# Kernel tuning notes

Measured on AMD Instinct MI355X. Metric: run time of the kernel, lower is better.

Reference implementation:

```python
import jax, jax.numpy as jnp
import numpy as np

N_SAMPLES = 2 ** 15          # 32768
STEP = 256                   # transform_step_size
WIN = 2048                   # transform/synthesis window
N_FRAMES = N_SAMPLES // STEP # 128
N_COEFFS = WIN // 2 + 1      # 1025
DILATIONS = (1, 2, 4, 8, 16, 32, 64, 1)


def hann(n):
    return 0.5 - 0.5 * jnp.cos(2.0 * jnp.pi * jnp.arange(n, dtype=jnp.float32) / n)


def transform(audio):
    # audio: (B, 1, N) -> magnitude STFT (B, 1024, 128)
    x = audio[:, 0, :]
    x = jnp.pad(x, ((0, 0), (0, WIN - STEP)))  # pad so n_frames == N_SAMPLES // STEP
    idx = np.arange(N_FRAMES)[:, None] * STEP + np.arange(WIN)[None, :]
    frames = x[:, idx] * hann(WIN)
    spec = jnp.abs(jnp.fft.rfft(frames, norm='ortho'))   # (B, F, 1025)
    return spec[..., : N_COEFFS - 1].transpose(0, 2, 1)  # (B, 1024, F)


def conv1x1(x, w, b):
    # x: (B, I, T), w: (O, I, 1), b: (O,)
    return jnp.einsum('oi,bit->bot', w[:, :, 0], x) + b[None, :, None]


def anticausal_block(x, w, b, dilation):
    # kernel_size=2 anti-causal dilated conv: looks at t and t+dilation (pad future)
    x_fut = jnp.pad(x, ((0, 0), (0, 0), (0, dilation)))[:, :, dilation:]
    y = (jnp.einsum('oi,bit->bot', w[:, :, 0], x)
         + jnp.einsum('oi,bit->bot', w[:, :, 1], x_fut)
         + b[None, :, None])
    y = jax.nn.leaky_relu(y, 0.2)
    y = y + x
    # do_norm: per-example max-norm
    y = y / (jnp.max(jnp.abs(y), axis=(1, 2), keepdims=True) + 1e-8)
    return y


def upsample_with_holes(x, desired_size):
    # zero-stuffing upsample: out[..., ::step] = x
    b, c, t = x.shape
    step = desired_size // t
    out = jnp.zeros((b, c, desired_size), x.dtype)
    return out.at[:, :, ::step].set(x)


def freq_domain_resonance(coeffs):
    # coeffs: (1, C, 1025) in [0, 1); per-frame decay = repeated spectral multiply
    c = jnp.clip(coeffs, 0.0, 0.9999)
    exps = jnp.arange(1, N_FRAMES + 1, dtype=coeffs.dtype)
    mags = c[:, :, None, :] ** exps[None, None, :, None]     # (1, C, F, 1025)
    frames = jnp.fft.irfft(mags, n=WIN) * hann(WIN)
    hop = WIN // 2
    total = hop * (N_FRAMES - 1) + WIN
    idx = np.arange(N_FRAMES)[:, None] * hop + np.arange(WIN)[None, :]
    out = jnp.zeros(frames.shape[:2] + (total,), frames.dtype)
    out = out.at[:, :, idx].add(frames)                      # overlap-add
    return out[..., :N_SAMPLES]                              # (1, C, N)


def fft_convolve(a, b):
    # circular-free conv via zero-padding to 2N, keep first N (matches repo fft_convolve)
    n = a.shape[-1]
    spec = jnp.fft.rfft(a, n=2 * n) * jnp.fft.rfft(b, n=2 * n)
    return jnp.fft.irfft(spec, n=2 * n)[..., :n]


def reference(audio, proj_in_w, proj_in_b, blocks_w, blocks_b,
              proj_sparse_w, proj_sparse_b, proj_dense_w, proj_dense_b, resonances):
    spec = transform(audio)                         # (B, 1024, 128)
    h = conv1x1(spec, proj_in_w, proj_in_b)         # (B, 32, 128)
    acc = jnp.zeros_like(h)
    for i, d in enumerate(DILATIONS):               # fixed 8-block stack
        h = anticausal_block(h, blocks_w[i], blocks_b[i], d)
        acc = acc + h
    x = conv1x1(acc, proj_sparse_w, proj_sparse_b)  # (B, 256, 128)
    sparse = jax.nn.relu(x)
    x = conv1x1(sparse, proj_dense_w, proj_dense_b) # (B, 32, 128)
    x = upsample_with_holes(x, N_SAMPLES)           # (B, 32, 32768)
    res = freq_domain_resonance(resonances)         # (1, 32, 32768), broadcast over B
    y = fft_convolve(x, res)                        # (B, 32, 32768)
    y = jnp.sum(y, axis=1, keepdims=True)           # (B, 1, 32768)
    return y, sparse


def setup_inputs() -> dict:
    key = jax.random.key(0)
    ks = jax.random.split(key, 12)
    u = lambda k, shape: jax.random.uniform(k, shape, jnp.float32, -0.05, 0.05)
    return {
        'audio': jax.random.normal(ks[0], (32, 1, N_SAMPLES), jnp.float32),
        'proj_in_w': u(ks[1], (32, 1024, 1)),
        'proj_in_b': jnp.zeros((32,), jnp.float32),
        'blocks_w': u(ks[2], (8, 32, 32, 2)),
        'blocks_b': jnp.zeros((8, 32), jnp.float32),
        'proj_sparse_w': u(ks[3], (256, 32, 1)),
        'proj_sparse_b': jnp.zeros((256,), jnp.float32),
        'proj_dense_w': u(ks[4], (32, 256, 1)),
        'proj_dense_b': jnp.zeros((32,), jnp.float32),
        'resonances': jax.random.uniform(ks[5], (1, 32, N_COEFFS), jnp.float32, 0.0, 1.0),
    }
```

## Files before the change

kernel.cpp:

```cpp
#include <hip/hip_runtime.h>

#define PI_F 3.14159265358979323846f

typedef short bf16x8 __attribute__((ext_vector_type(8)));
typedef float f32x4 __attribute__((ext_vector_type(4)));

#define MFMA16(acc, a, b) \
  acc = __builtin_amdgcn_mfma_f32_16x16x32_bf16(a, b, acc, 0, 0, 0)

#define WS_SPEC   0u
#define WS_H0     4194304u
#define WS_ACC    4325376u
#define WS_V      4456448u
#define WS_WTIN   4587520u
#define WS_WST    4620288u
#define WS_WDT    4628480u
#define WS_FRAMES 4636672u
#define WS_RES    6733824u

__device__ __forceinline__ void fft2048_stages(float2* buf, int tid) {
  for (int stage = 0; stage < 11; ++stage) {
    int half = 1 << stage;
    float base = -PI_F / (float)half;
    for (int t = tid; t < 1024; t += 256) {
      int j  = t & (half - 1);
      int i0 = ((t >> stage) << (stage + 1)) + j;
      int i1 = i0 + half;
      float s, c;
      __sincosf(base * (float)j, &s, &c);
      float2 u = buf[i0];
      float2 w = buf[i1];
      float tr = c * w.x - s * w.y;
      float ti = c * w.y + s * w.x;
      buf[i0] = make_float2(u.x + tr, u.y + ti);
      buf[i1] = make_float2(u.x - tr, u.y - ti);
    }
    __syncthreads();
  }
}

__global__ __launch_bounds__(256) void k_fft(const float* __restrict__ audio,
                                             const float* __restrict__ resin,
                                             float* __restrict__ spec,
                                             float* __restrict__ frames) {
  __shared__ float2 buf[2048];
  int blk = blockIdx.x;
  if (blk < 2048) {
    int b  = blk >> 6;
    int f0 = (blk & 63) * 2;
    for (int j = threadIdx.x; j < 2048; j += 256) {
      float h = 0.5f - 0.5f * __cosf(0.0030679615757712823f * (float)j);
      int i1 = f0 * 256 + j;
      int i2 = i1 + 256;
      float a1 = (i1 < 32768) ? audio[b * 32768 + i1] : 0.f;
      float a2 = (i2 < 32768) ? audio[b * 32768 + i2] : 0.f;
      buf[__brev((unsigned)j) >> 21] = make_float2(a1 * h, a2 * h);
    }
    __syncthreads();
    fft2048_stages(buf, threadIdx.x);
    const float scale = 0.5f * 0.022097086912079608f;
    for (int k = threadIdx.x; k < 1024; k += 256) {
      float2 zk = buf[k];
      float2 zn = buf[(2048 - k) & 2047];
      float f1r = zk.x + zn.x, f1i = zk.y - zn.y;
      float f2r = zk.y + zn.y, f2i = zk.x - zn.x;
      spec[(b * 128 + f0) * 1024 + k]     = sqrtf(f1r * f1r + f1i * f1i) * scale;
      spec[(b * 128 + f0 + 1) * 1024 + k] = sqrtf(f2r * f2r + f2i * f2i) * scale;
    }
  } else {
    int r = blk - 2048;
    int c = r >> 4;
    int g = r & 15;
    float e1 = (float)(2 * g + 1);
    for (int k = threadIdx.x; k < 2048; k += 256) {
      int kk = (k <= 1024) ? k : 2048 - k;
      float cv = resin[c * 1025 + kk];
      cv = fminf(fmaxf(cv, 0.f), 0.9999f);
      float m1 = __powf(cv, e1);
      float m2 = m1 * cv;
      buf[__brev((unsigned)k) >> 21] = make_float2(m1, m2);
    }
    __syncthreads();
    fft2048_stages(buf, threadIdx.x);
    for (int j = threadIdx.x; j < 2048; j += 256) {
      float h  = 0.5f - 0.5f * __cosf(0.0030679615757712823f * (float)j);
      float sc = h * (1.f / 2048.f);
      float2 z = buf[j];
      frames[(c * 32 + 2 * g) * 2048 + j]     = z.x * sc;
      frames[(c * 32 + 2 * g + 1) * 2048 + j] = z.y * sc;
    }
  }
}

__global__ __launch_bounds__(256) void k_prep(const float* __restrict__ Win,
                                              const float* __restrict__ Ws,
                                              const float* __restrict__ Wd,
                                              const float* __restrict__ bwIn,
                                              float* __restrict__ WT,
                                              float* __restrict__ WsT,
                                              float* __restrict__ WdT,
                                              short* __restrict__ Whg,
                                              short* __restrict__ Wlg) {
  int i = blockIdx.x * 256 + threadIdx.x;
  if (i < 32768) { int o = i >> 10, k = i & 1023; WT[k * 32 + o] = Win[i]; }
  if (i < 8192)  { int o2 = i >> 5, m = i & 31;   WsT[m * 256 + o2] = Ws[i]; }
  if (i < 8192)  { int c = i >> 8, o2 = i & 255;  WdT[o2 * 32 + c] = Wd[i]; }
  if (i < 16384) {
    int w = i & 1, m = (i >> 1) & 31, o = (i >> 6) & 31, s = i >> 11;
    float val = bwIn[i];
    unsigned bits = __float_as_uint(val);
    float rem = val - __uint_as_float(bits & 0xffff0000u);
    int row = (s * 2 + w) * 32 + o;
    Whg[row * 32 + m] = (short)(bits >> 16);
    Wlg[row * 32 + m] = (short)(__float_as_uint(rem) >> 16);
  }
}

__global__ __launch_bounds__(256) void k_proj_in(const float* __restrict__ spec,
                                                 const float* __restrict__ WT,
                                                 const float* __restrict__ bias,
                                                 float* __restrict__ h0) {
  __shared__ float specL[8][1024];
  __shared__ float red[32][8][8];
  int b  = blockIdx.x >> 4;
  int t0 = (blockIdx.x & 15) * 8;
  for (int i = threadIdx.x; i < 8192; i += 256) {
    int tt = i >> 10, k = i & 1023;
    specL[tt][k] = spec[(b * 128 + t0 + tt) * 1024 + k];
  }
  __syncthreads();
  int o = threadIdx.x & 31, p = threadIdx.x >> 5;
  float part[8] = {0.f,0.f,0.f,0.f,0.f,0.f,0.f,0.f};
  for (int i = 0; i < 128; ++i) {
    int k = p * 128 + ((i + p * 4) & 127);
    float w = WT[k * 32 + o];
#pragma unroll
    for (int tt = 0; tt < 8; ++tt) part[tt] += w * specL[tt][k];
  }
#pragma unroll
  for (int tt = 0; tt < 8; ++tt) red[o][tt][p] = part[tt];
  __syncthreads();
  int oo = threadIdx.x >> 3, tt2 = threadIdx.x & 7;
  float s = bias[oo];
#pragma unroll
  for (int p2 = 0; p2 < 8; ++p2) s += red[oo][tt2][p2];
  h0[b * 4096 + oo * 128 + t0 + tt2] = s;
}

__global__ __launch_bounds__(1024) void k_chain(const float* __restrict__ h0,
                                                const short* __restrict__ Whg,
                                                const short* __restrict__ Wlg,
                                                const float* __restrict__ bb,
                                                float* __restrict__ accout) {
  __shared__ __align__(16) short Hh[192 * 40];
  __shared__ __align__(16) short Hl[192 * 40];
  __shared__ float Hf[128 * 33];
  __shared__ float bL[256];
  __shared__ float red[16];
  int b = blockIdx.x, tid = threadIdx.x;

  for (int i = tid; i < 4096; i += 1024) {
    int t = i & 127;
    int o = i >> 7;
    float val = h0[b * 4096 + i];
    Hf[t * 33 + o] = val;
    unsigned bits = __float_as_uint(val);
    float rem = val - __uint_as_float(bits & 0xffff0000u);
    Hh[t * 40 + o] = (short)(bits >> 16);
    Hl[t * 40 + o] = (short)(__float_as_uint(rem) >> 16);
  }
  for (int i = tid; i < 64 * 40; i += 1024) {
    Hh[128 * 40 + i] = 0;
    Hl[128 * 40 + i] = 0;
  }
  if (tid < 256) bL[tid] = bb[tid];
  __syncthreads();

  int wave = tid >> 6, lane = tid & 63;
  int quad = lane >> 4, l15 = lane & 15;
  int t0 = (wave & 7) * 16, o0 = (wave >> 3) * 16;
  int tD = t0 + quad * 4;
  int oD = o0 + l15;

  const bf16x8* Hh8 = (const bf16x8*)Hh;
  const bf16x8* Hl8 = (const bf16x8*)Hl;
  const bf16x8* Wh8 = (const bf16x8*)Whg;
  const bf16x8* Wl8 = (const bf16x8*)Wlg;

  float accsum[4] = {0.f, 0.f, 0.f, 0.f};
  const int DIL[8] = {1, 2, 4, 8, 16, 32, 64, 1};

#pragma unroll
  for (int s = 0; s < 8; ++s) {
    int arow = t0 + l15;
    int frow = arow + DIL[s];
    bf16x8 Ah = Hh8[arow * 5 + quad];
    bf16x8 Al = Hl8[arow * 5 + quad];
    bf16x8 Fh = Hh8[frow * 5 + quad];
    bf16x8 Fl = Hl8[frow * 5 + quad];
    int w0row = ((s * 2 + 0) * 32 + oD) * 4 + quad;
    int w1row = ((s * 2 + 1) * 32 + oD) * 4 + quad;
    bf16x8 B0h = Wh8[w0row], B0l = Wl8[w0row];
    bf16x8 B1h = Wh8[w1row], B1l = Wl8[w1row];
    float bias = bL[s * 32 + oD];
    f32x4 acc = {bias, bias, bias, bias};
    MFMA16(acc, Ah, B0h); MFMA16(acc, Ah, B0l); MFMA16(acc, Al, B0h);
    MFMA16(acc, Fh, B1h); MFMA16(acc, Fh, B1l); MFMA16(acc, Fl, B1h);
    float hnew[4], lmax = 0.f;
#pragma unroll
    for (int r = 0; r < 4; ++r) {
      float sv = acc[r];
      sv = (sv > 0.f) ? sv : 0.2f * sv;
      sv += Hf[(tD + r) * 33 + oD];
      hnew[r] = sv;
      lmax = fmaxf(lmax, fabsf(sv));
    }
#pragma unroll
    for (int off = 32; off > 0; off >>= 1)
      lmax = fmaxf(lmax, __shfl_down(lmax, off, 64));
    if (lane == 0) red[wave] = lmax;
    __syncthreads();
    float mx = red[0];
#pragma unroll
    for (int i = 1; i < 16; ++i) mx = fmaxf(mx, red[i]);
    float nm = 1.f / (mx + 1e-8f);
#pragma unroll
    for (int r = 0; r < 4; ++r) {
      float hv = hnew[r] * nm;
      accsum[r] += hv;
      int t = tD + r;
      Hf[t * 33 + oD] = hv;
      unsigned bits = __float_as_uint(hv);
      float rem = hv - __uint_as_float(bits & 0xffff0000u);
      Hh[t * 40 + oD] = (short)(bits >> 16);
      Hl[t * 40 + oD] = (short)(__float_as_uint(rem) >> 16);
    }
    __syncthreads();
  }
#pragma unroll
  for (int r = 0; r < 4; ++r)
    accout[b * 4096 + (tD + r) * 32 + oD] = accsum[r];
}

__global__ __launch_bounds__(256) void k_sparse_dense(const float* __restrict__ acc,
                                                      const float* __restrict__ WsT,
                                                      const float* __restrict__ bs,
                                                      const float* __restrict__ WdT,
                                                      const float* __restrict__ bd,
                                                      float* __restrict__ out_sparse,
                                                      float* __restrict__ v) {
  __shared__ float accL[32];
  __shared__ float sL[256];
  __shared__ float red[8][32];
  int b = blockIdx.x >> 7, t = blockIdx.x & 127;
  int tid = threadIdx.x;
  if (tid < 32) accL[tid] = acc[b * 4096 + t * 32 + tid];
  __syncthreads();
  float s = bs[tid];
  for (int m = 0; m < 32; ++m) s += WsT[m * 256 + tid] * accL[m];
  s = fmaxf(s, 0.f);
  out_sparse[b * 32768 + tid * 128 + t] = s;
  sL[tid] = s;
  __syncthreads();
  int c = tid & 31, p = tid >> 5;
  float part = 0.f;
  for (int j = 0; j < 32; ++j) {
    int o2 = p * 32 + j;
    part += WdT[o2 * 32 + c] * sL[o2];
  }
  red[p][c] = part;
  __syncthreads();
  if (tid < 32) {
    float vv = bd[tid];
    for (int p2 = 0; p2 < 8; ++p2) vv += red[p2][tid];
    v[b * 4096 + tid * 128 + t] = vv;
  }
}

__global__ __launch_bounds__(256) void k_res_assemble(const float* __restrict__ frames,
                                                      float* __restrict__ res) {
  int i = blockIdx.x * 256 + threadIdx.x;
  int c = i >> 15, s = i & 32767;
  int g = s >> 10, j0 = s & 1023;
  float v = frames[(c * 32 + g) * 2048 + j0];
  if (g > 0) v += frames[(c * 32 + g - 1) * 2048 + j0 + 1024];
  res[i] = v;
}

__global__ __launch_bounds__(256) void k_bpack(const float* __restrict__ res,
                                               short* __restrict__ Bh,
                                               short* __restrict__ Bl) {
  int c = blockIdx.x >> 4, o = blockIdx.x & 15;
  int r = threadIdx.x;
  bf16x8 hv, lv;
#pragma unroll
  for (int j = 0; j < 8; ++j) {
    float val = res[c * 32768 + (8 * o + j) * 256 + r];
    unsigned bits = __float_as_uint(val);
    float rem = val - __uint_as_float(bits & 0xffff0000u);
    hv[j] = (short)(bits >> 16);
    lv[j] = (short)(__float_as_uint(rem) >> 16);
  }
  int unit = (blockIdx.x * 16 + (r >> 4)) * 16 + (r & 15);
  ((bf16x8*)Bh)[unit] = hv;
  ((bf16x8*)Bl)[unit] = lv;
}

__global__ __launch_bounds__(256, 2) void k_conv(const float* __restrict__ v,
                                                 const short* __restrict__ Bh,
                                                 const short* __restrict__ Bl,
                                                 float* __restrict__ y) {
  __shared__ __align__(16) short AH[2 * 32 * 264];
  __shared__ __align__(16) short AL[2 * 32 * 264];
  __shared__ float vwin[2][2][16][48];

  int blk = blockIdx.x;
  int b2 = blk / 20;
  int e  = blk - b2 * 20;
  int j, uc;
  if      (e < 2)  { j = 0; uc = e; }
  else if (e < 6)  { j = 1; uc = e - 2; }
  else if (e < 12) { j = 2; uc = e - 6; }
  else             { j = 3; uc = e - 12; }
  int D0 = 32 * j - 16 * uc;

  for (int i = threadIdx.x; i < 3008; i += 256) {
    int ii = i % 47;
    int r  = i / 47;
    int c  = r & 15, p = (r >> 4) & 1, bbv = r >> 5;
    int d  = D0 - 15 + ii;
    vwin[bbv][p][c][ii] = (d >= 0 && d < 128)
        ? v[(2 * b2 + bbv) * 4096 + (16 * p + c) * 128 + d] : 0.f;
  }
  __syncthreads();

  int lane = threadIdx.x & 63, wave = threadIdx.x >> 6;
  int quad = lane >> 4, l15 = lane & 15;
  int cq   = quad >> 1;
  int og   = 2 * uc + (quad & 1);
  int nt0  = wave * 4;

  f32x4 acc[4][4];
#pragma unroll
  for (int a = 0; a < 4; ++a)
#pragma unroll
    for (int t = 0; t < 4; ++t) acc[a][t] = (f32x4)0.f;

  const bf16x8* AH8 = (const bf16x8*)AH;
  const bf16x8* AL8 = (const bf16x8*)AL;
  const bf16x8* Bh8 = (const bf16x8*)Bh;
  const bf16x8* Bl8 = (const bf16x8*)Bl;
  short2* AH2 = (short2*)AH;
  short2* AL2 = (short2*)AL;

  int abase[4];
#pragma unroll
  for (int bbi = 0; bbi < 2; ++bbi)
#pragma unroll
    for (int qs = 0; qs < 2; ++qs)
      abase[bbi * 2 + qs] = (bbi * 32 + qs * 16 + l15) * 33 + quad;

  for (int p = 0; p < 2; ++p) {
    for (int i = threadIdx.x; i < 8192; i += 256) {
      int kk2 = i & 127;
      int row = (i >> 7) & 31;
      int bbv = i >> 12;
      int cl  = kk2 >> 3;
      int uu  = (kk2 & 7) * 2;
      int ii  = row - uu + 15;
      float v0 = vwin[bbv][p][cl][ii];
      float v1 = vwin[bbv][p][cl][ii - 1];
      unsigned w0 = __float_as_uint(v0), w1 = __float_as_uint(v1);
      float r0 = v0 - __uint_as_float(w0 & 0xffff0000u);
      float r1 = v1 - __uint_as_float(w1 & 0xffff0000u);
      int u2 = (bbv * 32 + row) * 132 + kk2;
      AH2[u2] = make_short2((short)(w0 >> 16), (short)(w1 >> 16));
      AL2[u2] = make_short2((short)(__float_as_uint(r0) >> 16),
                            (short)(__float_as_uint(r1) >> 16));
    }
    __syncthreads();

#pragma unroll
    for (int ks = 0; ks < 8; ++ks) {
      bf16x8 ah[4], al[4];
#pragma unroll
      for (int tl = 0; tl < 4; ++tl) {
        ah[tl] = AH8[abase[tl] + ks * 4];
        al[tl] = AL8[abase[tl] + ks * 4];
      }
      int c = 16 * p + 2 * ks + cq;
      int bb0 = (c * 16 + og) * 256 + l15;
#pragma unroll
      for (int t = 0; t < 4; ++t) {
        int bi = bb0 + (nt0 + t) * 16;
        bf16x8 bvh = Bh8[bi];
        bf16x8 bvl = Bl8[bi];
#pragma unroll
        for (int tl = 0; tl < 4; ++tl) {
          MFMA16(acc[tl][t], ah[tl], bvh);
          MFMA16(acc[tl][t], ah[tl], bvl);
          MFMA16(acc[tl][t], al[tl], bvh);
        }
      }
    }
    __syncthreads();
  }

#pragma unroll
  for (int bbi = 0; bbi < 2; ++bbi)
#pragma unroll
    for (int qs = 0; qs < 2; ++qs) {
      float* yb = y + (2 * b2 + bbi) * 32768
                    + (32 * j + qs * 16 + quad * 4) * 256 + l15;
#pragma unroll
      for (int t = 0; t < 4; ++t)
#pragma unroll
        for (int reg = 0; reg < 4; ++reg)
          atomicAdd(yb + reg * 256 + (nt0 + t) * 16, acc[bbi * 2 + qs][t][reg]);
    }
}

extern "C" void kernel_launch(void* const* d_in, const int* in_sizes, int n_in,
                              void* d_out, int out_size, void* d_ws, size_t ws_size,
                              hipStream_t stream) {
  const float* audio = (const float*)d_in[0];
  const float* Win   = (const float*)d_in[1];
  const float* bin   = (const float*)d_in[2];
  const float* bw    = (const float*)d_in[3];
  const float* bb    = (const float*)d_in[4];
  const float* Ws    = (const float*)d_in[5];
  const float* bs    = (const float*)d_in[6];
  const float* Wd    = (const float*)d_in[7];
  const float* bd    = (const float*)d_in[8];
  const float* reson = (const float*)d_in[9];

  float* out = (float*)d_out;
  float* ws  = (float*)d_ws;

  float* spec   = ws + WS_SPEC;
  float* h0     = ws + WS_H0;
  float* accb   = ws + WS_ACC;
  float* vbuf   = ws + WS_V;
  float* WT     = ws + WS_WTIN;
  float* WsT    = ws + WS_WST;
  float* WdT    = ws + WS_WDT;
  float* frames = ws + WS_FRAMES;
  float* resbuf = ws + WS_RES;
  short* Bh = (short*)(ws + WS_FRAMES);
  short* Bl = (short*)(ws + WS_FRAMES + 524288u);
  short* Whg = (short*)(ws + WS_V);
  short* Wlg = (short*)(ws + WS_V + 8192u);

  hipMemsetAsync(d_out, 0, 1048576u * sizeof(float), stream);

  k_prep<<<128, 256, 0, stream>>>(Win, Ws, Wd, bw, WT, WsT, WdT, Whg, Wlg);
  k_fft<<<2560, 256, 0, stream>>>(audio, reson, spec, frames);
  k_res_assemble<<<4096, 256, 0, stream>>>(frames, resbuf);
  k_bpack<<<512, 256, 0, stream>>>(resbuf, Bh, Bl);
  k_proj_in<<<512, 256, 0, stream>>>(spec, WT, bin, h0);
  k_chain<<<32, 1024, 0, stream>>>(h0, Whg, Wlg, bb, accb);
  k_sparse_dense<<<4096, 256, 0, stream>>>(accb, WsT, bs, WdT, bd, out + 1048576, vbuf);
  k_conv<<<320, 256, 0, stream>>>(vbuf, Bh, Bl, out);
}
```

Baseline: 215.2 us.

## Split k_conv per batch with 8 waves and smaller per-wave tiles

Each k_conv block now handles one batch element instead of a pair, using 512 threads where each wave computes a 2x2 MFMA tile instead of 4x4. The grid doubles to 640 blocks, and LDS and register use per block drop, to raise occupancy and parallelism across CUs. The trade-off is that each B fragment loaded from global memory is reused across fewer A tiles and fewer batches, so B traffic per FLOP doubles and the number of atomic adds stays about the same.

```diff
diff --git a/kernel.cpp b/kernel.cpp
--- a/kernel.cpp
+++ b/kernel.cpp
@@ -306,17 +306,17 @@
   ((bf16x8*)Bl)[unit] = lv;
 }
 
-__global__ __launch_bounds__(256, 2) void k_conv(const float* __restrict__ v,
+__global__ __launch_bounds__(512, 4) void k_conv(const float* __restrict__ v,
                                                  const short* __restrict__ Bh,
                                                  const short* __restrict__ Bl,
                                                  float* __restrict__ y) {
-  __shared__ __align__(16) short AH[2 * 32 * 264];
-  __shared__ __align__(16) short AL[2 * 32 * 264];
-  __shared__ float vwin[2][2][16][48];
+  __shared__ __align__(16) short AH[32 * 264];
+  __shared__ __align__(16) short AL[32 * 264];
+  __shared__ float vwin[2][16][48];
 
   int blk = blockIdx.x;
-  int b2 = blk / 20;
-  int e  = blk - b2 * 20;
+  int b = blk / 20;
+  int e = blk - b * 20;
   int j, uc;
   if      (e < 2)  { j = 0; uc = e; }
   else if (e < 6)  { j = 1; uc = e - 2; }
@@ -324,13 +324,13 @@
   else             { j = 3; uc = e - 12; }
   int D0 = 32 * j - 16 * uc;
 
-  for (int i = threadIdx.x; i < 3008; i += 256) {
+  for (int i = threadIdx.x; i < 1504; i += 512) {
     int ii = i % 47;
     int r  = i / 47;
-    int c  = r & 15, p = (r >> 4) & 1, bbv = r >> 5;
+    int c  = r & 15, p = r >> 4;
     int d  = D0 - 15 + ii;
-    vwin[bbv][p][c][ii] = (d >= 0 && d < 128)
-        ? v[(2 * b2 + bbv) * 4096 + (16 * p + c) * 128 + d] : 0.f;
+    vwin[p][c][ii] = (d >= 0 && d < 128)
+        ? v[b * 4096 + (16 * p + c) * 128 + d] : 0.f;
   }
   __syncthreads();
 
@@ -338,13 +338,10 @@
   int quad = lane >> 4, l15 = lane & 15;
   int cq   = quad >> 1;
   int og   = 2 * uc + (quad & 1);
-  int nt0  = wave * 4;
-
-  f32x4 acc[4][4];
-#pragma unroll
-  for (int a = 0; a < 4; ++a)
-#pragma unroll
-    for (int t = 0; t < 4; ++t) acc[a][t] = (f32x4)0.f;
+  int nt0  = wave * 2;
+
+  f32x4 acc00 = (f32x4)0.f, acc01 = (f32x4)0.f;
+  f32x4 acc10 = (f32x4)0.f, acc11 = (f32x4)0.f;
 
   const bf16x8* AH8 = (const bf16x8*)AH;
   const bf16x8* AL8 = (const bf16x8*)AL;
@@ -353,27 +350,22 @@
   short2* AH2 = (short2*)AH;
   short2* AL2 = (short2*)AL;
 
-  int abase[4];
-#pragma unroll
-  for (int bbi = 0; bbi < 2; ++bbi)
-#pragma unroll
-    for (int qs = 0; qs < 2; ++qs)
-      abase[bbi * 2 + qs] = (bbi * 32 + qs * 16 + l15) * 33 + quad;
+  int abase0 = (0 * 16 + l15) * 33 + quad;
+  int abase1 = (1 * 16 + l15) * 33 + quad;
 
   for (int p = 0; p < 2; ++p) {
-    for (int i = threadIdx.x; i < 8192; i += 256) {
+    for (int i = threadIdx.x; i < 4096; i += 512) {
       int kk2 = i & 127;
-      int row = (i >> 7) & 31;
-      int bbv = i >> 12;
+      int row = i >> 7;
       int cl  = kk2 >> 3;
       int uu  = (kk2 & 7) * 2;
       int ii  = row - uu + 15;
-      float v0 = vwin[bbv][p][cl][ii];
-      float v1 = vwin[bbv][p][cl][ii - 1];
+      float v0 = vwin[p][cl][ii];
+      float v1 = vwin[p][cl][ii - 1];
       unsigned w0 = __float_as_uint(v0), w1 = __float_as_uint(v1);
       float r0 = v0 - __uint_as_float(w0 & 0xffff0000u);
       float r1 = v1 - __uint_as_float(w1 & 0xffff0000u);
-      int u2 = (bbv * 32 + row) * 132 + kk2;
+      int u2 = row * 132 + kk2;
       AH2[u2] = make_short2((short)(w0 >> 16), (short)(w1 >> 16));
       AL2[u2] = make_short2((short)(__float_as_uint(r0) >> 16),
                             (short)(__float_as_uint(r1) >> 16));
@@ -382,42 +374,35 @@
 
 #pragma unroll
     for (int ks = 0; ks < 8; ++ks) {
-      bf16x8 ah[4], al[4];
-#pragma unroll
-      for (int tl = 0; tl < 4; ++tl) {
-        ah[tl] = AH8[abase[tl] + ks * 4];
-        al[tl] = AL8[abase[tl] + ks * 4];
-      }
-      int c = 16 * p + 2 * ks + cq;
+      bf16x8 ah0 = AH8[abase0 + ks * 4];
+      bf16x8 al0 = AL8[abase0 + ks * 4];
+      bf16x8 ah1 = AH8[abase1 + ks * 4];
+      bf16x8 al1 = AL8[abase1 + ks * 4];
+      int c   = 16 * p + 2 * ks + cq;
       int bb0 = (c * 16 + og) * 256 + l15;
-#pragma unroll
-      for (int t = 0; t < 4; ++t) {
-        int bi = bb0 + (nt0 + t) * 16;
-        bf16x8 bvh = Bh8[bi];
-        bf16x8 bvl = Bl8[bi];
-#pragma unroll
-        for (int tl = 0; tl < 4; ++tl) {
-          MFMA16(acc[tl][t], ah[tl], bvh);
-          MFMA16(acc[tl][t], ah[tl], bvl);
-          MFMA16(acc[tl][t], al[tl], bvh);
-        }
-      }
-    }
-    __syncthreads();
-  }
-
-#pragma unroll
-  for (int bbi = 0; bbi < 2; ++bbi)
-#pragma unroll
-    for (int qs = 0; qs < 2; ++qs) {
-      float* yb = y + (2 * b2 + bbi) * 32768
-                    + (32 * j + qs * 16 + quad * 4) * 256 + l15;
-#pragma unroll
-      for (int t = 0; t < 4; ++t)
-#pragma unroll
-        for (int reg = 0; reg < 4; ++reg)
-          atomicAdd(yb + reg * 256 + (nt0 + t) * 16, acc[bbi * 2 + qs][t][reg]);
-    }
+      bf16x8 bh0 = Bh8[bb0 + nt0 * 16];
+      bf16x8 bl0 = Bl8[bb0 + nt0 * 16];
+      bf16x8 bh1 = Bh8[bb0 + (nt0 + 1) * 16];
+      bf16x8 bl1 = Bl8[bb0 + (nt0 + 1) * 16];
+      MFMA16(acc00, ah0, bh0); MFMA16(acc00, ah0, bl0); MFMA16(acc00, al0, bh0);
+      MFMA16(acc10, ah1, bh0); MFMA16(acc10, ah1, bl0); MFMA16(acc10, al1, bh0);
+      MFMA16(acc01, ah0, bh1); MFMA16(acc01, ah0, bl1); MFMA16(acc01, al0, bh1);
+      MFMA16(acc11, ah1, bh1); MFMA16(acc11, ah1, bl1); MFMA16(acc11, al1, bh1);
+    }
+    __syncthreads();
+  }
+
+  {
+    float* yb0 = y + b * 32768 + (32 * j + 0 * 16 + quad * 4) * 256 + l15;
+    float* yb1 = y + b * 32768 + (32 * j + 1 * 16 + quad * 4) * 256 + l15;
+#pragma unroll
+    for (int reg = 0; reg < 4; ++reg) {
+      atomicAdd(yb0 + reg * 256 + (nt0 + 0) * 16, acc00[reg]);
+      atomicAdd(yb0 + reg * 256 + (nt0 + 1) * 16, acc01[reg]);
+      atomicAdd(yb1 + reg * 256 + (nt0 + 0) * 16, acc10[reg]);
+      atomicAdd(yb1 + reg * 256 + (nt0 + 1) * 16, acc11[reg]);
+    }
+  }
 }
 
 extern "C" void kernel_launch(void* const* d_in, const int* in_sizes, int n_in,
@@ -460,5 +445,5 @@
   k_proj_in<<<512, 256, 0, stream>>>(spec, WT, bin, h0);
   k_chain<<<32, 1024, 0, stream>>>(h0, Whg, Wlg, bb, accb);
   k_sparse_dense<<<4096, 256, 0, stream>>>(accb, WsT, bs, WdT, bd, out + 1048576, vbuf);
-  k_conv<<<320, 256, 0, stream>>>(vbuf, Bh, Bl, out);
-}
+  k_conv<<<640, 512, 0, stream>>>(vbuf, Bh, Bl, out);
+}
```

Measured after the change: 202.7 us. 1.06x faster.
